# Kernel optimization log

Hardware: AMD Instinct MI355X
Metric: run time of the kernel (lower is better)

The kernel has to match this reference:

```python
import jax, jax.numpy as jnp
import numpy as np

B, NPG, T, F, H, C, O = 16, 256, 8, 64, 64, 32, 64
N = B * NPG
E = 65536
EPS = 1e-15

def setup_inputs():
    key = jax.random.key(0)
    ks = jax.random.split(key, 12)
    pos = jax.random.normal(ks[0], (N, T, F), jnp.float32)
    g = jax.random.randint(ks[1], (E,), 0, B)
    src = g * NPG + jax.random.randint(ks[2], (E,), 0, NPG)
    dst = g * NPG + jax.random.randint(ks[3], (E,), 0, NPG)
    edge_index = jnp.stack([src, dst])
    edge_attr = jax.random.uniform(ks[4], (E,), jnp.float32)
    batch = jnp.repeat(jnp.arange(B), NPG)
    w = lambda k, s: jax.random.normal(k, s, jnp.float32) * 0.05
    return dict(
        pos=pos, edge_index=edge_index, edge_attr=edge_attr, batch=batch,
        W1=w(ks[5], (F, H)), b1=jnp.zeros((H,), jnp.float32),
        p1W=w(ks[6], (H, 2 * C)), p1b=jnp.zeros((2 * C,), jnp.float32),
        c2rW=w(ks[7], (H, H)), c2rb=jnp.zeros((H,), jnp.float32),
        c2sW=w(ks[8], (H, H)),
        p2W=w(ks[9], (H, C)), p2b=jnp.zeros((C,), jnp.float32),
        c3rW=w(ks[10], (H, O)), c3rb=jnp.zeros((O,), jnp.float32),
        c3sW=w(ks[11], (H, O)),
    )

def _gcn_conv(x, row, col, ew, W, b):
    # GCNConv with edge weights: add self loops (w=1), symmetric norm, x@W, scatter-add.
    loop = jnp.arange(N)
    r = jnp.concatenate([row, loop])
    c = jnp.concatenate([col, loop])
    w = jnp.concatenate([ew, jnp.ones((N,), ew.dtype)])
    deg = jax.ops.segment_sum(w, c, num_segments=N)
    dinv = jnp.where(deg > 0, jax.lax.rsqrt(jnp.where(deg > 0, deg, 1.0)), 0.0)
    norm = dinv[r] * w * dinv[c]
    xw = x @ W  # [N,T,H]
    out = jax.ops.segment_sum(xw[r] * norm[:, None, None], c, num_segments=N)
    return out + b

def _dense_graph_conv(x, adj, Wr, br, Ws):
    # DenseGraphConv(aggr='add'): lin_rel(adj @ x) + lin_root(x)
    return jnp.einsum('bnm,btmh->btnh', adj, x) @ Wr + br + x @ Ws

def _mincut_pool(x, adj, s, mask=None):
    # x [B,T,n,H], adj [B,n,n], s logits [B,n,k]
    s = jax.nn.softmax(s, axis=-1)
    if mask is not None:
        m = mask.astype(x.dtype)
        x = x * m[:, None, :, None]
        s = s * m[:, :, None]
    out = jnp.einsum('bnk,btnh->btkh', s, x)
    out_adj = jnp.einsum('bnk,bnm,bmj->bkj', s, adj, s)
    mincut_num = jnp.trace(out_adj, axis1=1, axis2=2)
    d_flat = adj.sum(axis=-1)  # degree vector
    mincut_den = jnp.einsum('bnk,bn,bnk->b', s, d_flat, s)  # trace(S^T D S)
    mincut_loss = jnp.mean(-(mincut_num / mincut_den))
    k = s.shape[-1]
    ss = jnp.einsum('bnk,bnj->bkj', s, s)
    ss_fro = jnp.sqrt(jnp.sum(ss * ss, axis=(1, 2), keepdims=True))
    tgt = jnp.eye(k, dtype=x.dtype) / jnp.sqrt(jnp.asarray(k, x.dtype))
    ortho_loss = jnp.mean(jnp.sqrt(jnp.sum((ss / ss_fro - tgt) ** 2, axis=(1, 2))))
    ind = jnp.arange(k)
    out_adj = out_adj.at[:, ind, ind].set(0.0)
    d = jnp.sqrt(out_adj.sum(axis=-1))[:, None] + EPS  # [B,1,k]
    out_adj = (out_adj / d) / jnp.swapaxes(d, 1, 2)
    return out, out_adj, mincut_loss, ortho_loss

def _forward(pos, edge_attr, W1, b1, p1W, p1b, c2rW, c2rb, c2sW, p2W, p2b, c3rW, c3rb, c3sW, edge_index, batch):
    row, col = edge_index[0], edge_index[1]
    h = jax.nn.relu(_gcn_conv(pos, row, col, edge_attr, W1, b1))  # [N,T,H]
    # to_dense_batch / to_dense_adj
    counts = jax.ops.segment_sum(jnp.ones((N,), jnp.int32), batch, num_segments=B)
    offsets = jnp.cumsum(counts) - counts
    pin = jnp.arange(N) - offsets[batch]  # index within graph
    xd = jnp.zeros((B, NPG, T, H), h.dtype).at[batch, pin].set(h)
    mask = jnp.zeros((B, NPG), bool).at[batch, pin].set(True)
    adj = jnp.zeros((B, NPG, NPG), h.dtype).at[batch[row], pin[row], pin[col]].add(1.0)
    x = jnp.swapaxes(xd, 1, 2)  # [B,T,n,H]
    s1 = jnp.tanh((x @ p1W + p1b).mean(axis=1))  # [B,n,2C]
    x, adj, mc1, o1 = _mincut_pool(x, adj, s1, mask)
    x = jax.nn.relu(_dense_graph_conv(x, adj, c2rW, c2rb, c2sW))  # [B,T,2C,H]
    s2 = jnp.tanh((x @ p2W + p2b).mean(axis=1))  # [B,2C,C]
    x, adj, mc2, o2 = _mincut_pool(x, adj, s2, None)
    x = _dense_graph_conv(x, adj, c3rW, c3rb, c3sW)  # [B,T,C,O]
    agg = jnp.einsum('bnc,bck->bnk', jax.nn.softmax(s1, axis=-1), jax.nn.softmax(s2, axis=-1))
    return x, mc1 + mc2, o1 + o2, agg

def reference(pos, edge_index, edge_attr, batch, W1, b1, p1W, p1b, c2rW, c2rb, c2sW, p2W, p2b, c3rW, c3rb, c3sW):
    return _forward(pos, edge_attr, W1, b1, p1W, p1b, c2rW, c2rb, c2sW, p2W, p2b, c3rW, c3rb, c3sW, edge_index, batch)
```

## Files before the change

kernel.cpp:

```cpp
#include <hip/hip_runtime.h>
#include <cstdint>


#define WS_WADJT 0
#define WS_ADN   1048576
#define WS_WSUM  2097152
#define WS_XW    2101248
#define WS_H     4198400
#define WS_S1    6295552
#define WS_TMP   6557696
#define WS_DFLAT 6819840
#define WS_ADJ1  6823936
#define WS_X1    6889472
#define WS_X2    7413760
#define WS_S2    8200192
#define WS_ADJ2  8232960
#define WS_SCAL  8249344

__device__ __forceinline__ float blockRedSum16(float v, float* red) {
  #pragma unroll
  for (int m = 32; m; m >>= 1) v += __shfl_xor(v, m);
  __syncthreads();
  if ((threadIdx.x & 63) == 0) red[threadIdx.x >> 6] = v;
  __syncthreads();
  float s = 0.f;
  #pragma unroll
  for (int i = 0; i < 16; ++i) s += red[i];
  __syncthreads();
  return s;
}

__global__ __launch_bounds__(1024) void k_p0(const float* __restrict__ pos,
                                             const int* __restrict__ ei,
                                             const float* __restrict__ ea,
                                             const float* __restrict__ W1,
                                             float* __restrict__ ws) {
  __shared__ float sm[4096];
  int tid = threadIdx.x, blk = blockIdx.x;
  for (int i = tid; i < 4096; i += 1024) sm[i] = W1[i];
  __syncthreads();
  int col = tid & 63;
  #pragma unroll
  for (int pass = 0; pass < 8; ++pass) {
    int row = blk * 128 + pass * 16 + (tid >> 6);
    const float* a = pos + (size_t)row * 64;
    float acc = 0.f;
    #pragma unroll 8
    for (int k = 0; k < 64; ++k) acc += a[k] * sm[k * 64 + col];
    ws[WS_XW + (size_t)row * 64 + col] = acc;
  }
  if (tid < 256) {
    int e = blk * 256 + tid;
    int s = ei[e], d = ei[65536 + e];
    int g = s >> 8, r = s & 255, c = d & 255;
    float w = ea[e];
    atomicAdd(&ws[WS_WADJT + (size_t)(((g << 8) + c) << 8) + r], w);
    atomicAdd(&ws[WS_ADN + (size_t)(((g << 8) + r) << 8) + c], 1.0f);
    atomicAdd(&ws[WS_WSUM + (g << 8) + c], w);
  }
}

__global__ __launch_bounds__(1024) void k_gcn_s1(float* __restrict__ ws,
                                                 const float* __restrict__ b1,
                                                 const float* __restrict__ p1W,
                                                 const float* __restrict__ p1b) {
  __shared__ float sm[7696];
  int tid = threadIdx.x, blk = blockIdx.x;
  float* sW = sm;
  float* dinvL = sm + 4096;
  float* pL = sm + 4352;
  float* red4 = sm + 5376;
  float* xm = sm + 6400;
  int* iL = (int*)(sm + 6656);
  int* wcnt = (int*)(sm + 7680);
  int g = blk >> 4;
  for (int i = tid; i < 4096; i += 1024) sW[i] = p1W[i];
  if (tid < 256) dinvL[tid] = rsqrtf(ws[WS_WSUM + (g << 8) + tid] + 1.0f);
  __syncthreads();
  int ng = tid >> 8, ltid = tid & 255, lw = (tid >> 6) & 3, lane = tid & 63;
  float bb = b1[ltid & 63];
  for (int it = 0; it < 4; ++it) {
    int n = blk * 16 + it * 4 + ng;
    int cc = n & 255;
    float dn = dinvL[cc];
    float pv = ws[WS_WADJT + (size_t)n * 256 + ltid] * dinvL[ltid] * dn;
    if (ltid == cc) pv += dn * dn;
    bool act = (pv != 0.f);
    unsigned long long mask = __ballot(act);
    int wpos = (int)__popcll(mask & ((1ull << lane) - 1ull));
    if (lane == 0) wcnt[ng * 4 + lw] = (int)__popcll(mask);
    __syncthreads();
    int base = 0;
    #pragma unroll
    for (int i = 0; i < 4; ++i) base += (i < lw) ? wcnt[ng * 4 + i] : 0;
    int na = wcnt[ng * 4] + wcnt[ng * 4 + 1] + wcnt[ng * 4 + 2] + wcnt[ng * 4 + 3];
    if (act) { iL[ng * 256 + base + wpos] = ltid; pL[ng * 256 + base + wpos] = pv; }
    __syncthreads();
    const float* xg = ws + WS_XW + (size_t)g * 131072;
    float acc0 = 0.f, acc1 = 0.f;
    #pragma unroll 4
    for (int i = 0; i < na; ++i) {
      int r = iL[ng * 256 + i];
      float p = pL[ng * 256 + i];
      acc0 += p * xg[(size_t)r * 512 + ltid];
      acc1 += p * xg[(size_t)r * 512 + 256 + ltid];
    }
    acc0 = fmaxf(acc0 + bb, 0.f);
    acc1 = fmaxf(acc1 + bb, 0.f);
    float* hp = ws + WS_H + (size_t)n * 512;
    hp[ltid] = acc0;
    hp[256 + ltid] = acc1;
    red4[ng * 256 + lw * 64 + (ltid & 63)] = acc0 + acc1;
    __syncthreads();
    if (ltid < 64) {
      xm[ng * 64 + ltid] = 0.125f * (red4[ng * 256 + ltid] + red4[ng * 256 + 64 + ltid] +
                                     red4[ng * 256 + 128 + ltid] + red4[ng * 256 + 192 + ltid]);
      float a = p1b[ltid];
      #pragma unroll 4
      for (int kq = 0; kq < 64; ++kq) a += xm[ng * 64 + kq] * sW[kq * 64 + ltid];
      float v = tanhf(a);
      float mx = v;
      #pragma unroll
      for (int m = 32; m; m >>= 1) mx = fmaxf(mx, __shfl_xor(mx, m));
      float e = __expf(v - mx);
      float se = e;
      #pragma unroll
      for (int m = 32; m; m >>= 1) se += __shfl_xor(se, m);
      ws[WS_S1 + (size_t)n * 64 + ltid] = e / se;
    }
    __syncthreads();
  }
}

__global__ __launch_bounds__(1024) void k_as1(float* __restrict__ ws) {
  __shared__ float sm[8192];
  int tid = threadIdx.x, blk = blockIdx.x;
  float* aL = sm;
  int* iLa = (int*)(sm + 4096);
  int w = tid >> 6, lane = tid & 63;
  int n = blk * 16 + w;
  int g = n >> 8;
  float4 av = *(const float4*)(ws + WS_ADN + (size_t)n * 256 + lane * 4);
  float rs = av.x + av.y + av.z + av.w;
  #pragma unroll
  for (int m = 32; m; m >>= 1) rs += __shfl_xor(rs, m);
  if (lane == 0) ws[WS_DFLAT + n] = rs;
  float avv[4] = {av.x, av.y, av.z, av.w};
  unsigned long long below = (1ull << lane) - 1ull;
  int base = 0;
  #pragma unroll
  for (int q = 0; q < 4; ++q) {
    bool act = (avv[q] != 0.f);
    unsigned long long mask = __ballot(act);
    if (act) {
      int p = base + (int)__popcll(mask & below);
      iLa[w * 256 + p] = lane * 4 + q;
      aL[w * 256 + p] = avv[q];
    }
    base += (int)__popcll(mask);
  }
  int na = base;
  float acc = 0.f;
  const float* S1g = ws + WS_S1 + ((size_t)g << 8) * 64;
  #pragma unroll 4
  for (int i = 0; i < na; ++i) {
    int m = iLa[w * 256 + i];
    float a = aL[w * 256 + i];
    acc += a * S1g[(size_t)m * 64 + lane];
  }
  ws[WS_TMP + (size_t)n * 64 + lane] = acc;
}

__global__ __launch_bounds__(1024) void k_pool1x1(float* __restrict__ ws) {
  __shared__ float sm[5328];
  int tid = threadIdx.x, blk = blockIdx.x;
  if (blk < 16) {
    int b = blk;
    float* S1c = sm;
    float* Tc = sm + 2048;
    float* prs = sm + 4096;
    float* diagL = sm + 5184;
    float* dd = sm + 5248;
    float* red = sm + 5312;
    const float* Sb = ws + WS_S1 + (size_t)b * 16384;
    const float* Tb = ws + WS_TMP + (size_t)b * 16384;
    int k = tid >> 4, j0 = (tid & 15) * 4;
    float accA[4] = {0, 0, 0, 0}, accS[4] = {0, 0, 0, 0};
    for (int n0 = 0; n0 < 256; n0 += 32) {
      __syncthreads();
      S1c[tid] = Sb[n0 * 64 + tid];
      S1c[tid + 1024] = Sb[n0 * 64 + 1024 + tid];
      Tc[tid] = Tb[n0 * 64 + tid];
      Tc[tid + 1024] = Tb[n0 * 64 + 1024 + tid];
      __syncthreads();
      for (int i = 0; i < 32; ++i) {
        float sk = S1c[i * 64 + k];
        float4 tv = *(const float4*)(Tc + i * 64 + j0);
        float4 sv = *(const float4*)(S1c + i * 64 + j0);
        accA[0] += sk * tv.x; accA[1] += sk * tv.y; accA[2] += sk * tv.z; accA[3] += sk * tv.w;
        accS[0] += sk * sv.x; accS[1] += sk * sv.y; accS[2] += sk * sv.z; accS[3] += sk * sv.w;
      }
    }
    float num = 0.f, fro2 = 0.f, rsp = 0.f;
    #pragma unroll
    for (int q = 0; q < 4; ++q) { rsp += accA[q]; fro2 += accS[q] * accS[q]; }
    if (k >= j0 && k < j0 + 4) { num = accA[k - j0]; diagL[k] = accA[k - j0]; }
    prs[k * 17 + (tid & 15)] = rsp;
    __syncthreads();
    if (tid < 64) {
      float rs = 0.f;
      #pragma unroll
      for (int i = 0; i < 16; ++i) rs += prs[tid * 17 + i];
      dd[tid] = sqrtf(fmaxf(rs - diagL[tid], 0.f)) + 1e-15f;
    }
    float denp = 0.f;
    if (tid < 256) {
      const float* s = Sb + tid * 64;
      float qq = 0.f;
      for (int kk = 0; kk < 64; kk += 4) {
        float4 v = *(const float4*)(s + kk);
        qq += v.x * v.x + v.y * v.y + v.z * v.z + v.w * v.w;
      }
      denp = qq * ws[WS_DFLAT + (b << 8) + tid];
    }
    float numT = blockRedSum16(num, red);
    float denT = blockRedSum16(denp, red);
    float froT = sqrtf(blockRedSum16(fro2, red));
    float inv_fro = 1.f / froT;
    float osum = 0.f;
    #pragma unroll
    for (int q = 0; q < 4; ++q) {
      float v = accS[q] * inv_fro - ((j0 + q) == k ? 0.125f : 0.f);
      osum += v * v;
    }
    float orT = blockRedSum16(osum, red);
    float* adj = ws + WS_ADJ1 + (size_t)b * 4096;
    float dk = dd[k];
    #pragma unroll
    for (int q = 0; q < 4; ++q) {
      int j = j0 + q;
      adj[k * 64 + j] = (k == j) ? 0.f : accA[q] / (dk * dd[j]);
    }
    if (tid == 0) {
      ws[WS_SCAL + b] = numT / denT;
      ws[WS_SCAL + 16 + b] = sqrtf(orT);
    }
  } else {
    int bt = blk - 16;
    int b = bt >> 3, t = bt & 7;
    int hc = tid & 63, kb = (tid >> 6) * 4;
    float* sS = sm;
    float* sX = sm + 2048;
    float acc[4] = {0, 0, 0, 0};
    for (int n0 = 0; n0 < 256; n0 += 32) {
      __syncthreads();
      for (int idx = tid; idx < 2048; idx += 1024) {
        int i = idx >> 6, c = idx & 63;
        sS[idx] = ws[WS_S1 + ((size_t)((b << 8) + n0 + i)) * 64 + c];
        sX[idx] = ws[WS_H + ((size_t)((b << 8) + n0 + i)) * 512 + t * 64 + c];
      }
      __syncthreads();
      for (int i = 0; i < 32; ++i) {
        float xv = sX[i * 64 + hc];
        #pragma unroll
        for (int q = 0; q < 4; ++q) acc[q] += sS[i * 64 + kb + q] * xv;
      }
    }
    #pragma unroll
    for (int q = 0; q < 4; ++q)
      ws[WS_X1 + ((size_t)bt * 64 + kb + q) * 64 + hc] = acc[q];
  }
}

__global__ __launch_bounds__(1024) void k_conv2(float* __restrict__ ws,
                                                const float* __restrict__ c2rW,
                                                const float* __restrict__ c2rb,
                                                const float* __restrict__ c2sW) {
  __shared__ float sm[20800];
  int tid = threadIdx.x, blk = blockIdx.x;
  int bt = blk;
  int b = bt >> 3;
  float* sA = sm;
  float* sX = sm + 4160;
  float* sY = sm + 8320;
  float* sWr = sm + 12480;
  float* sWs = sm + 16640;
  for (int idx = tid; idx < 4096; idx += 1024) {
    int r = idx >> 6, c = idx & 63;
    sA[r * 65 + c] = ws[WS_ADJ1 + (size_t)b * 4096 + idx];
    sX[r * 65 + c] = ws[WS_X1 + (size_t)bt * 4096 + idx];
    sWr[r * 65 + c] = c2rW[idx];
    sWs[r * 65 + c] = c2sW[idx];
  }
  __syncthreads();
  int n = tid >> 4, h0 = (tid & 15) * 4;
  float acc[4];
  #pragma unroll
  for (int q = 0; q < 4; ++q) acc[q] = 0.f;
  for (int m = 0; m < 64; ++m) {
    float a = sA[n * 65 + m];
    #pragma unroll
    for (int q = 0; q < 4; ++q) acc[q] += a * sX[m * 65 + h0 + q];
  }
  #pragma unroll
  for (int q = 0; q < 4; ++q) sY[n * 65 + h0 + q] = acc[q];
  __syncthreads();
  #pragma unroll
  for (int q = 0; q < 4; ++q) acc[q] = c2rb[h0 + q];
  for (int m = 0; m < 64; ++m) {
    float y = sY[n * 65 + m], x = sX[n * 65 + m];
    #pragma unroll
    for (int q = 0; q < 4; ++q)
      acc[q] += y * sWr[m * 65 + h0 + q] + x * sWs[m * 65 + h0 + q];
  }
  #pragma unroll
  for (int q = 0; q < 4; ++q)
    ws[WS_X2 + (size_t)bt * 4096 + n * 64 + h0 + q] = fmaxf(acc[q], 0.f);
}

__global__ __launch_bounds__(1024) void k_s2pool2(float* __restrict__ ws,
                                                  const float* __restrict__ p2W,
                                                  const float* __restrict__ p2b) {
  __shared__ float sm[16752];
  int tid = threadIdx.x;
  int b = blockIdx.x;
  float* xmL = sm;
  float* sS2 = sm + 4096;
  float* sA2 = sm + 6208;
  float* sT  = sm + 10368;
  float* oaL = sm + 12480;
  float* ssL = sm + 13536;
  float* sdf = sm + 14592;
  float* ddL = sm + 14656;
  float* red = sm + 14688;
  float* sp2W = sm + 14704;
  for (int idx = tid; idx < 4096; idx += 1024)
    sA2[(idx >> 6) * 65 + (idx & 63)] = ws[WS_ADJ1 + (size_t)b * 4096 + idx];
  for (int idx = tid; idx < 2048; idx += 1024) sp2W[idx] = p2W[idx];
  for (int idx = tid; idx < 4096; idx += 1024) {
    int n = idx >> 6, f = idx & 63;
    float s = 0.f;
    #pragma unroll
    for (int t = 0; t < 8; ++t)
      s += ws[WS_X2 + ((size_t)(b * 8 + t) * 64 + n) * 64 + f];
    xmL[idx] = s * 0.125f;
  }
  __syncthreads();
  {
    int n = tid >> 4, j0 = (tid & 15) * 2;
    float a0 = p2b[j0], a1 = p2b[j0 + 1];
    for (int kq = 0; kq < 64; ++kq) {
      float v = xmL[n * 64 + kq];
      a0 += v * sp2W[kq * 32 + j0];
      a1 += v * sp2W[kq * 32 + j0 + 1];
    }
    float v0 = tanhf(a0), v1 = tanhf(a1);
    float mx = fmaxf(v0, v1);
    #pragma unroll
    for (int off = 8; off; off >>= 1) mx = fmaxf(mx, __shfl_xor(mx, off));
    float e0 = __expf(v0 - mx), e1 = __expf(v1 - mx);
    float se = e0 + e1;
    #pragma unroll
    for (int off = 8; off; off >>= 1) se += __shfl_xor(se, off);
    float inv = 1.f / se;
    e0 *= inv; e1 *= inv;
    sS2[n * 33 + j0] = e0;
    sS2[n * 33 + j0 + 1] = e1;
    ws[WS_S2 + (size_t)(b * 64 + n) * 32 + j0] = e0;
    ws[WS_S2 + (size_t)(b * 64 + n) * 32 + j0 + 1] = e1;
  }
  __syncthreads();
  if (tid < 64) {
    float s = 0.f;
    for (int m = 0; m < 64; ++m) s += sA2[tid * 65 + m];
    sdf[tid] = s;
  }
  {
    int n2 = tid >> 4, j0 = (tid & 15) * 2;
    float t0 = 0.f, t1 = 0.f;
    for (int m = 0; m < 64; ++m) {
      float a = sA2[n2 * 65 + m];
      t0 += a * sS2[m * 33 + j0];
      t1 += a * sS2[m * 33 + j0 + 1];
    }
    sT[n2 * 33 + j0] = t0;
    sT[n2 * 33 + j0 + 1] = t1;
  }
  float accD = 0.f;
  if (tid < 64) {
    float t = 0.f;
    for (int q = 0; q < 32; ++q) { float v = sS2[tid * 33 + q]; t += v * v; }
    accD = t * sdf[tid];
  }
  __syncthreads();
  int k5 = tid >> 5, j5 = tid & 31;
  float accA = 0.f, accS = 0.f;
  for (int n3 = 0; n3 < 64; ++n3) {
    float sk = sS2[n3 * 33 + k5];
    accA += sk * sT[n3 * 33 + j5];
    accS += sk * sS2[n3 * 33 + j5];
  }
  oaL[k5 * 33 + j5] = accA;
  ssL[k5 * 33 + j5] = accS;
  float fro2p = accS * accS;
  __syncthreads();
  float num = 0.f, trs = 0.f;
  if (tid < 32) {
    num = oaL[tid * 33 + tid];
    trs = ssL[tid * 33 + tid];
    float rs = 0.f;
    for (int j = 0; j < 32; ++j) rs += oaL[tid * 33 + j];
    ddL[tid] = sqrtf(fmaxf(rs - num, 0.f)) + 1e-15f;
  }
  float numT = blockRedSum16(num, red);
  float denT = blockRedSum16(accD, red);
  float froT = sqrtf(blockRedSum16(fro2p, red));
  float trT = blockRedSum16(trs, red);
  {
    float dk = ddL[k5];
    float* a2 = ws + WS_ADJ2 + (size_t)b * 1024;
    a2[k5 * 32 + j5] = (k5 == j5) ? 0.f : oaL[k5 * 33 + j5] / (dk * ddL[j5]);
  }
  if (tid == 0) {
    ws[WS_SCAL + 32 + b] = numT / denT;
    ws[WS_SCAL + 48 + b] = sqrtf(fmaxf(2.f - 2.f * trT / (5.656854249f * froT), 0.f));
  }
}

__global__ __launch_bounds__(1024) void k_final(float* __restrict__ ws,
                                                const float* __restrict__ c3rW,
                                                const float* __restrict__ c3rb,
                                                const float* __restrict__ c3sW,
                                                float* __restrict__ out) {
  __shared__ float sm[19808];
  int tid = threadIdx.x, blk = blockIdx.x;
  if (blk < 128) {
    int bt = blk, b = bt >> 3;
    float* sX  = sm;
    float* sS  = sm + 4160;
    float* sX3 = sm + 6272;
    float* sA  = sm + 8352;
    float* sY  = sm + 9408;
    float* sWr = sm + 11488;
    float* sWs = sm + 15648;
    for (int idx = tid; idx < 4096; idx += 1024)
      sX[(idx >> 6) * 65 + (idx & 63)] = ws[WS_X2 + (size_t)bt * 4096 + idx];
    for (int idx = tid; idx < 2048; idx += 1024)
      sS[(idx >> 5) * 33 + (idx & 31)] = ws[WS_S2 + (size_t)b * 2048 + idx];
    sA[(tid >> 5) * 33 + (tid & 31)] = ws[WS_ADJ2 + (size_t)b * 1024 + tid];
    for (int idx = tid; idx < 4096; idx += 1024) {
      int r = idx >> 6, c = idx & 63;
      sWr[r * 65 + c] = c3rW[idx];
      sWs[r * 65 + c] = c3sW[idx];
    }
    __syncthreads();
    int k = tid >> 5, h0 = (tid & 31) * 2;
    float a0 = 0.f, a1 = 0.f;
    for (int n = 0; n < 64; ++n) {
      float sv = sS[n * 33 + k];
      a0 += sv * sX[n * 65 + h0];
      a1 += sv * sX[n * 65 + h0 + 1];
    }
    sX3[k * 65 + h0] = a0;
    sX3[k * 65 + h0 + 1] = a1;
    __syncthreads();
    a0 = 0.f; a1 = 0.f;
    for (int m = 0; m < 32; ++m) {
      float a = sA[k * 33 + m];
      a0 += a * sX3[m * 65 + h0];
      a1 += a * sX3[m * 65 + h0 + 1];
    }
    sY[k * 65 + h0] = a0;
    sY[k * 65 + h0 + 1] = a1;
    __syncthreads();
    a0 = c3rb[h0]; a1 = c3rb[h0 + 1];
    for (int m = 0; m < 64; ++m) {
      float y = sY[k * 65 + m], x = sX3[k * 65 + m];
      a0 += y * sWr[m * 65 + h0] + x * sWs[m * 65 + h0];
      a1 += y * sWr[m * 65 + h0 + 1] + x * sWs[m * 65 + h0 + 1];
    }
    out[(size_t)bt * 2048 + k * 64 + h0] = a0;
    out[(size_t)bt * 2048 + k * 64 + h0 + 1] = a1;
  } else {
    int rb = blk - 128;
    int b = rb >> 3, sub = rb & 7;
    float* sS = sm;
    for (int idx = tid; idx < 2048; idx += 1024)
      sS[(idx >> 5) * 33 + (idx & 31)] = ws[WS_S2 + (size_t)b * 2048 + idx];
    __syncthreads();
    int n = sub * 32 + (tid >> 5), j = tid & 31;
    const float* s1r = ws + WS_S1 + ((size_t)((b << 8) + n)) * 64;
    float acc = 0.f;
    #pragma unroll 4
    for (int kq = 0; kq < 64; ++kq) acc += s1r[kq] * sS[kq * 33 + j];
    out[262146 + ((size_t)((b << 8) + n)) * 32 + j] = acc;
    if (blk == 255 && tid == 0) {
      float mc = 0.f, o = 0.f;
      #pragma unroll
      for (int b2 = 0; b2 < 16; ++b2) {
        mc += ws[WS_SCAL + b2] + ws[WS_SCAL + 32 + b2];
        o += ws[WS_SCAL + 16 + b2] + ws[WS_SCAL + 48 + b2];
      }
      out[262144] = -mc / 16.0f;
      out[262145] = o / 16.0f;
    }
  }
}

extern "C" void kernel_launch(void* const* d_in, const int* in_sizes, int n_in,
                              void* d_out, int out_size, void* d_ws, size_t ws_size,
                              hipStream_t stream) {
  (void)in_sizes; (void)n_in; (void)out_size; (void)ws_size;
  const float* pos = (const float*)d_in[0];
  const int* ei = (const int*)d_in[1];
  const float* ea = (const float*)d_in[2];
  const float* W1 = (const float*)d_in[4];
  const float* b1 = (const float*)d_in[5];
  const float* p1W = (const float*)d_in[6];
  const float* p1b = (const float*)d_in[7];
  const float* c2rW = (const float*)d_in[8];
  const float* c2rb = (const float*)d_in[9];
  const float* c2sW = (const float*)d_in[10];
  const float* p2W = (const float*)d_in[11];
  const float* p2b = (const float*)d_in[12];
  const float* c3rW = (const float*)d_in[13];
  const float* c3rb = (const float*)d_in[14];
  const float* c3sW = (const float*)d_in[15];
  float* ws = (float*)d_ws;
  float* out = (float*)d_out;

  hipMemsetAsync(d_ws, 0, (size_t)2101248 * sizeof(float), stream);
  k_p0<<<dim3(256), dim3(1024), 0, stream>>>(pos, ei, ea, W1, ws);
  k_gcn_s1<<<dim3(256), dim3(1024), 0, stream>>>(ws, b1, p1W, p1b);
  k_as1<<<dim3(256), dim3(1024), 0, stream>>>(ws);
  k_pool1x1<<<dim3(144), dim3(1024), 0, stream>>>(ws);
  k_conv2<<<dim3(128), dim3(1024), 0, stream>>>(ws, c2rW, c2rb, c2sW);
  k_s2pool2<<<dim3(16), dim3(1024), 0, stream>>>(ws, p2W, p2b);
  k_final<<<dim3(256), dim3(1024), 0, stream>>>(ws, c3rW, c3rb, c3sW, out);
}
```

Measured before the change: 261.2 us.

## Fuse sparse adjacency-times-S1 kernel into pool1 kernel via shared memory

Removes the separate k_as1 launch and computes adj@S1 and row degrees inside the first 16 blocks of k_pool1x1, keeping the intermediate in LDS instead of global workspace. This saves a kernel launch and the global write and read of the intermediate. In exchange, that work now runs on only 16 blocks (each wave processes 16 rows serially) instead of 256 blocks, so parallelism drops and LDS per block grows to about 97KB.

```diff
diff --git a/kernel.cpp b/kernel.cpp
--- a/kernel.cpp
+++ b/kernel.cpp
@@ -8,8 +8,6 @@
 #define WS_XW    2101248
 #define WS_H     4198400
 #define WS_S1    6295552
-#define WS_TMP   6557696
-#define WS_DFLAT 6819840
 #define WS_ADJ1  6823936
 #define WS_X1    6889472
 #define WS_X2    7413760
@@ -132,70 +130,69 @@
   }
 }
 
-__global__ __launch_bounds__(1024) void k_as1(float* __restrict__ ws) {
-  __shared__ float sm[8192];
-  int tid = threadIdx.x, blk = blockIdx.x;
-  float* aL = sm;
-  int* iLa = (int*)(sm + 4096);
-  int w = tid >> 6, lane = tid & 63;
-  int n = blk * 16 + w;
-  int g = n >> 8;
-  float4 av = *(const float4*)(ws + WS_ADN + (size_t)n * 256 + lane * 4);
-  float rs = av.x + av.y + av.z + av.w;
-  #pragma unroll
-  for (int m = 32; m; m >>= 1) rs += __shfl_xor(rs, m);
-  if (lane == 0) ws[WS_DFLAT + n] = rs;
-  float avv[4] = {av.x, av.y, av.z, av.w};
-  unsigned long long below = (1ull << lane) - 1ull;
-  int base = 0;
-  #pragma unroll
-  for (int q = 0; q < 4; ++q) {
-    bool act = (avv[q] != 0.f);
-    unsigned long long mask = __ballot(act);
-    if (act) {
-      int p = base + (int)__popcll(mask & below);
-      iLa[w * 256 + p] = lane * 4 + q;
-      aL[w * 256 + p] = avv[q];
-    }
-    base += (int)__popcll(mask);
-  }
-  int na = base;
-  float acc = 0.f;
-  const float* S1g = ws + WS_S1 + ((size_t)g << 8) * 64;
-  #pragma unroll 4
-  for (int i = 0; i < na; ++i) {
-    int m = iLa[w * 256 + i];
-    float a = aL[w * 256 + i];
-    acc += a * S1g[(size_t)m * 64 + lane];
-  }
-  ws[WS_TMP + (size_t)n * 64 + lane] = acc;
-}
-
 __global__ __launch_bounds__(1024) void k_pool1x1(float* __restrict__ ws) {
-  __shared__ float sm[5328];
+  __shared__ float sm[24832];
   int tid = threadIdx.x, blk = blockIdx.x;
   if (blk < 16) {
     int b = blk;
-    float* S1c = sm;
-    float* Tc = sm + 2048;
-    float* prs = sm + 4096;
-    float* diagL = sm + 5184;
-    float* dd = sm + 5248;
-    float* red = sm + 5312;
+    float* TMPc = sm;
+    float* dfL  = sm + 16384;
+    float* scr  = sm + 16640;
+    int w = tid >> 6, lane = tid & 63;
+    {
+      float* aL = scr;
+      int* iLa = (int*)(scr + 4096);
+      const float* S1g = ws + WS_S1 + ((size_t)b << 8) * 64;
+      for (int i = 0; i < 16; ++i) {
+        int nl = w * 16 + i;
+        int n = (b << 8) + nl;
+        float4 av = *(const float4*)(ws + WS_ADN + (size_t)n * 256 + lane * 4);
+        float rs = av.x + av.y + av.z + av.w;
+        #pragma unroll
+        for (int m = 32; m; m >>= 1) rs += __shfl_xor(rs, m);
+        if (lane == 0) dfL[nl] = rs;
+        float avv[4] = {av.x, av.y, av.z, av.w};
+        unsigned long long below = (1ull << lane) - 1ull;
+        int base = 0;
+        #pragma unroll
+        for (int q = 0; q < 4; ++q) {
+          bool act = (avv[q] != 0.f);
+          unsigned long long mask = __ballot(act);
+          if (act) {
+            int p = base + (int)__popcll(mask & below);
+            iLa[w * 256 + p] = lane * 4 + q;
+            aL[w * 256 + p] = avv[q];
+          }
+          base += (int)__popcll(mask);
+        }
+        int na = base;
+        float acc = 0.f;
+        #pragma unroll 4
+        for (int i2 = 0; i2 < na; ++i2) {
+          int m = iLa[w * 256 + i2];
+          float a = aL[w * 256 + i2];
+          acc += a * S1g[(size_t)m * 64 + lane];
+        }
+        TMPc[nl * 64 + lane] = acc;
+      }
+    }
+    __syncthreads();
+    float* S1c = scr;
+    float* prs = scr + 2048;
+    float* diagL = scr + 3136;
+    float* dd = scr + 3200;
+    float* red = scr + 3264;
     const float* Sb = ws + WS_S1 + (size_t)b * 16384;
-    const float* Tb = ws + WS_TMP + (size_t)b * 16384;
     int k = tid >> 4, j0 = (tid & 15) * 4;
     float accA[4] = {0, 0, 0, 0}, accS[4] = {0, 0, 0, 0};
     for (int n0 = 0; n0 < 256; n0 += 32) {
       __syncthreads();
       S1c[tid] = Sb[n0 * 64 + tid];
       S1c[tid + 1024] = Sb[n0 * 64 + 1024 + tid];
-      Tc[tid] = Tb[n0 * 64 + tid];
-      Tc[tid + 1024] = Tb[n0 * 64 + 1024 + tid];
       __syncthreads();
       for (int i = 0; i < 32; ++i) {
         float sk = S1c[i * 64 + k];
-        float4 tv = *(const float4*)(Tc + i * 64 + j0);
+        float4 tv = *(const float4*)(TMPc + (n0 + i) * 64 + j0);
         float4 sv = *(const float4*)(S1c + i * 64 + j0);
         accA[0] += sk * tv.x; accA[1] += sk * tv.y; accA[2] += sk * tv.z; accA[3] += sk * tv.w;
         accS[0] += sk * sv.x; accS[1] += sk * sv.y; accS[2] += sk * sv.z; accS[3] += sk * sv.w;
@@ -221,7 +218,7 @@
         float4 v = *(const float4*)(s + kk);
         qq += v.x * v.x + v.y * v.y + v.z * v.z + v.w * v.w;
       }
-      denp = qq * ws[WS_DFLAT + (b << 8) + tid];
+      denp = qq * dfL[tid];
     }
     float numT = blockRedSum16(num, red);
     float denT = blockRedSum16(denp, red);
@@ -532,7 +529,6 @@
   hipMemsetAsync(d_ws, 0, (size_t)2101248 * sizeof(float), stream);
   k_p0<<<dim3(256), dim3(1024), 0, stream>>>(pos, ei, ea, W1, ws);
   k_gcn_s1<<<dim3(256), dim3(1024), 0, stream>>>(ws, b1, p1W, p1b);
-  k_as1<<<dim3(256), dim3(1024), 0, stream>>>(ws);
   k_pool1x1<<<dim3(144), dim3(1024), 0, stream>>>(ws);
   k_conv2<<<dim3(128), dim3(1024), 0, stream>>>(ws, c2rW, c2rb, c2sW);
   k_s2pool2<<<dim3(16), dim3(1024), 0, stream>>>(ws, p2W, p2b);
```

After: 292.5 us. 1.12x slower.
